# Performance work log

Hardware: AMD Instinct MI355X
Metric: run time of the kernel (lower is better)

## Reference

```python
import jax, jax.numpy as jnp
import numpy as np

THRESH = 0.5
DECAY = 0.99
D = 2048
K = 16384  # memory at full capacity -> static shapes


def _l2norm(x):
    return x / jnp.linalg.norm(x, axis=1, keepdims=True)


def _compute_logits(z, prototypes, temp):
    # temp * <z_hat, p_hat>  -> [1, K]
    return temp[0] * (_l2norm(z) @ _l2norm(prototypes).T)


def setup_inputs() -> dict:
    key = jax.random.key(0)
    k1, k2, k3 = jax.random.split(key, 3)
    z = jax.random.normal(k1, (1, D), dtype=jnp.float32)
    prototypes = jax.random.normal(k2, (K, D), dtype=jnp.float32)
    usages = jax.random.uniform(k3, (K, 1), dtype=jnp.float32, minval=0.1, maxval=1.0)
    beta = jnp.array([-12.0], dtype=jnp.float32)
    gamma = jnp.array([1.0], dtype=jnp.float32)
    temp = jnp.array([10.0], dtype=jnp.float32)
    return {"z": z, "prototypes": prototypes, "usages": usages,
            "beta": beta, "gamma": gamma, "temp": temp}


def reference(z, prototypes, usages, beta, gamma, temp):
    # --- similarity + novelty gate ---
    logits = _compute_logits(z, prototypes, temp)            # [1, K]
    u = jax.nn.sigmoid((-jax.lax.stop_gradient(jnp.max(logits)) - beta[0]) / gamma[0])  # scalar

    def evict_branch(_):
        # remove least-used prototype, append z at the end (shapes stay [K, .])
        idx = jnp.argmin(usages[:, 0])
        pos = jnp.arange(K - 1)
        src = jnp.where(pos < idx, pos, pos + 1)             # skip row idx
        new_p = jnp.concatenate([prototypes[src], z], axis=0)
        new_u = jnp.concatenate([usages[src], jnp.ones((1, 1), usages.dtype)], axis=0)
        return new_p, new_u

    def ema_branch(_):
        y = jax.nn.softmax(logits, axis=1)                   # [1, K]
        delta = (y * (1.0 - u)).T                            # [K, 1]
        new_p = z * (delta / (delta + usages)) + prototypes * (usages / (usages + delta))
        return new_p, usages + delta

    new_protos, new_usages = jax.lax.cond(u >= THRESH, evict_branch, ema_branch, None)
    new_usages = new_usages * DECAY

    # --- final logits / pseudo-label / self cross-entropy ---
    logits2 = _compute_logits(z, new_protos, temp)           # [1, K]
    label = jnp.argmax(logits2, axis=1)                      # [1]
    loss = -jax.nn.log_softmax(logits2, axis=1)[0, label[0]]
    return loss, label, u, new_protos, new_usages
```

## Files before the change

### kernel.cpp

```cpp
#include <hip/hip_runtime.h>
#include <math.h>

#define KP 16384
#define DP 2048
#define THRESH 0.5f
#define DECAY 0.99f


typedef float f4 __attribute__((ext_vector_type(4)));
typedef float f2 __attribute__((ext_vector_type(2)));
typedef unsigned long long u64;

__device__ __forceinline__ float waveReduceSum(float v) {
    #pragma unroll
    for (int m = 32; m >= 1; m >>= 1) v += __shfl_xor(v, m, 64);
    return v;
}

__device__ __forceinline__ unsigned int fkey(float v) {
    unsigned int b = __float_as_uint(v);
    return (b & 0x80000000u) ? ~b : (b | 0x80000000u);
}
__device__ __forceinline__ float fkey_inv(unsigned int key) {
    unsigned int b = (key & 0x80000000u) ? (key ^ 0x80000000u) : ~key;
    return __uint_as_float(b);
}

__global__ __launch_bounds__(1024) void k_argmin(const float* __restrict__ usages,
                                                 float* __restrict__ W) {
    __shared__ u64 s[16];
    const int t = threadIdx.x;
    u64 best = ~0ULL;
    #pragma unroll
    for (int i = 0; i < KP / 1024; i++) {
        const int j = t + i * 1024;
        u64 p = ((u64)fkey(usages[j]) << 32) | (unsigned int)j;
        if (p < best) best = p;
    }
    #pragma unroll
    for (int m = 32; m >= 1; m >>= 1) {
        u64 o = __shfl_xor(best, m, 64);
        if (o < best) best = o;
    }
    if ((t & 63) == 0) s[t >> 6] = best;
    __syncthreads();
    if (t < 64) {
        best = s[t & 15];
        #pragma unroll
        for (int m = 8; m >= 1; m >>= 1) {
            u64 o = __shfl_xor(best, m, 64);
            if (o < best) best = o;
        }
        if (t == 0) ((int*)W)[2] = (int)(best & 0xFFFFFFFFu);
    }
}

__global__ __launch_bounds__(256) void k_dots_copy(const float* __restrict__ z,
                                                   const float* __restrict__ P,
                                                   const float* __restrict__ temp,
                                                   float* __restrict__ W,
                                                   float* __restrict__ out) {
    const int wave = threadIdx.x >> 6;
    const int lane = threadIdx.x & 63;
    const int r = blockIdx.x * 4 + wave;
    const int idx = ((const int*)W)[2];

    const float* prow = P + (size_t)r * DP;

    f4 v[8];
    float zp = 0.f, pp = 0.f, zz = 0.f;
    #pragma unroll
    for (int i = 0; i < 8; i++) {
        const int c = i * 256 + lane * 4;
        const f4 pv = __builtin_nontemporal_load((const f4*)(prow + c));
        const f4 zv = *(const f4*)(z + c);
        v[i] = pv;
        zp += pv.x * zv.x + pv.y * zv.y + pv.z * zv.z + pv.w * zv.w;
        pp += pv.x * pv.x + pv.y * pv.y + pv.z * pv.z + pv.w * pv.w;
        zz += zv.x * zv.x + zv.y * zv.y + zv.z * zv.z + zv.w * zv.w;
    }

    if (r != idx) {
        const int ro = (r < idx) ? r : r - 1;
        float* orow = out + 3 + (size_t)ro * DP;
        if (lane == 0) __builtin_nontemporal_store(v[0].x, orow);
        #pragma unroll
        for (int i = 0; i < 8; i++) {
            float nx = __shfl_down(v[i].x, 1);
            const float bx = __shfl(v[(i + 1) & 7].x, 0);
            if (lane == 63) nx = bx;
            f4 ov;
            ov.x = v[i].y; ov.y = v[i].z; ov.z = v[i].w; ov.w = nx;
            if (i < 7 || lane < 63) {
                __builtin_nontemporal_store(ov, (f4*)(orow + 1 + 4 * (i * 64 + lane)));
            }
        }
        if (lane == 63) {
            f2 t2; t2.x = v[7].y; t2.y = v[7].z;
            __builtin_nontemporal_store(t2, (f2*)(orow + DP - 3));
            __builtin_nontemporal_store(v[7].w, orow + DP - 1);
        }
    }

    zp = waveReduceSum(zp);
    pp = waveReduceSum(pp);
    zz = waveReduceSum(zz);
    if (lane == 0) {
        W[8 + r]          = temp[0] * zp / sqrtf(zz * pp);
        W[8 + KP + r]     = zp;
        W[8 + 2 * KP + r] = pp;
        if (r == 0) W[7] = zz;
    }
}

__global__ __launch_bounds__(1024) void k_scalar(const float* __restrict__ z,
                                                 const float* __restrict__ usages,
                                                 const float* __restrict__ beta,
                                                 const float* __restrict__ gamma,
                                                 const float* __restrict__ temp,
                                                 float* __restrict__ W,
                                                 float* __restrict__ out) {
    __shared__ float sf[1024];
    __shared__ float sm[16];
    __shared__ u64 sb[16];
    const int t = threadIdx.x;
    const int idx = ((const int*)W)[2];

    float lg[KP / 1024];
    float mx_all = -INFINITY;
    u64 bestx = 0;
    #pragma unroll
    for (int i = 0; i < KP / 1024; i++) {
        const int j = t + i * 1024;
        const float v = W[8 + j];
        lg[i] = v;
        mx_all = fmaxf(mx_all, v);
        if (j != idx) {
            u64 p = ((u64)fkey(v) << 32) | (unsigned int)(~j);
            if (p > bestx) bestx = p;
        }
    }
    #pragma unroll
    for (int m = 32; m >= 1; m >>= 1) {
        mx_all = fmaxf(mx_all, __shfl_xor(mx_all, m, 64));
        u64 o = __shfl_xor(bestx, m, 64);
        if (o > bestx) bestx = o;
    }
    if ((t & 63) == 0) { sm[t >> 6] = mx_all; sb[t >> 6] = bestx; }
    __syncthreads();
    if (t < 64) {
        float m = sm[t & 15];
        u64 b = sb[t & 15];
        #pragma unroll
        for (int mk = 8; mk >= 1; mk >>= 1) {
            m = fmaxf(m, __shfl_xor(m, mk, 64));
            u64 o = __shfl_xor(b, mk, 64);
            if (o > b) b = o;
        }
        if (t == 0) { sm[0] = m; sb[0] = b; }
    }
    __syncthreads();
    mx_all = sm[0];

    const float u = 1.f / (1.f + expf(-((-mx_all - beta[0]) / gamma[0])));
    const int flag = (u >= THRESH) ? 1 : 0;
    if (t == 0) {
        out[2] = u;
        ((int*)W)[3] = flag;
        W[4] = mx_all;
        W[6] = u;
    }

    if (flag) {
        const u64 bp = sb[0];
        const float mxe = fkey_inv((unsigned int)(bp >> 32));
        const int amax = (int)(~(unsigned int)(bp & 0xFFFFFFFFu));

        const float tq = temp[0];
        const float M2 = fmaxf(mxe, tq);
        float s = 0.f;
        #pragma unroll
        for (int i = 0; i < KP / 1024; i++) {
            const int j = t + i * 1024;
            if (j != idx) s += expf(lg[i] - M2);
        }
        sf[t] = s;
        __syncthreads();
        for (int off = 512; off >= 1; off >>= 1) {
            if (t < off) sf[t] += sf[t + off];
            __syncthreads();
        }
        if (t == 0) {
            const float total = sf[0] + expf(tq - M2);
            out[0] = logf(total);
            const int label = (mxe >= tq) ? (amax < idx ? amax : amax - 1) : (KP - 1);
            out[1] = (float)label;
        }
        float* ou = out + 3 + (size_t)KP * DP;
        #pragma unroll
        for (int i = 0; i < KP / 1024; i++) {
            const int j = t + i * 1024;
            ou[j] = (j < KP - 1) ? usages[j < idx ? j : j + 1] * DECAY : DECAY;
        }
        float* orow = out + 3 + (size_t)(KP - 1) * DP;
        orow[t] = z[t];
        orow[t + 1024] = z[t + 1024];
    } else {
        float s = 0.f;
        #pragma unroll
        for (int i = 0; i < KP / 1024; i++) s += expf(lg[i] - mx_all);
        sf[t] = s;
        __syncthreads();
        for (int off = 512; off >= 1; off >>= 1) {
            if (t < off) sf[t] += sf[t + off];
            __syncthreads();
        }
        if (t == 0) W[5] = sf[0];
    }
}

__global__ __launch_bounds__(256) void k_ema(const float* __restrict__ z,
                                             const float* __restrict__ P,
                                             const float* __restrict__ usages,
                                             const float* __restrict__ temp,
                                             float* __restrict__ W,
                                             float* __restrict__ out) {
    if (((const int*)W)[3]) return;
    __shared__ float lds[4 * DP];
    const int wave = threadIdx.x >> 6;
    const int lane = threadIdx.x & 63;
    const int r = blockIdx.x * 4 + wave;

    const float mx = W[4], se = W[5], u = W[6], zz = W[7];
    const float lg = W[8 + r], zp = W[8 + KP + r], pp = W[8 + 2 * KP + r];
    const float y = expf(lg - mx) / se;
    const float delta = y * (1.f - u);
    const float usg = usages[r];
    const float a = delta / (delta + usg);
    const float b = usg / (usg + delta);

    const float* prow = P + (size_t)r * DP;
    float* wl = lds + wave * DP;
    float* orow = out + 3 + (size_t)r * DP;
    #pragma unroll
    for (int i = 0; i < 8; i++) {
        const int c = i * 256 + lane * 4;
        const float4 pv = *(const float4*)(prow + c);
        const float4 zv = *(const float4*)(z + c);
        float4 ov;
        ov.x = a * zv.x + b * pv.x;
        ov.y = a * zv.y + b * pv.y;
        ov.z = a * zv.z + b * pv.z;
        ov.w = a * zv.w + b * pv.w;
        *(float4*)(wl + c) = ov;
    }
    #pragma unroll
    for (int j = 0; j < DP / 64; j++) {
        orow[j * 64 + lane] = wl[j * 64 + lane];
    }
    if (lane == 0) {
        const float dzn = a * zz + b * zp;
        const float n2 = a * a * zz + 2.f * a * b * zp + b * b * pp;
        W[8 + 3 * KP + r] = temp[0] * dzn / sqrtf(zz * n2);
        out[3 + (size_t)KP * DP + r] = (usg + delta) * DECAY;
    }
}

__global__ __launch_bounds__(1024) void k_ema_loss(const float* __restrict__ W,
                                                   float* __restrict__ out) {
    if (((const int*)W)[3]) return;
    __shared__ unsigned long long sp[1024];
    __shared__ float sf[1024];
    const int t = threadIdx.x;

    float l2[KP / 1024];
    u64 best = 0;
    #pragma unroll
    for (int i = 0; i < KP / 1024; i++) {
        const int j = t + i * 1024;
        const float v = W[8 + 3 * KP + j];
        l2[i] = v;
        u64 p = ((u64)fkey(v) << 32) | (unsigned int)(~j);
        if (p > best) best = p;
    }
    sp[t] = best;
    __syncthreads();
    for (int off = 512; off >= 1; off >>= 1) {
        if (t < off) { if (sp[t + off] > sp[t]) sp[t] = sp[t + off]; }
        __syncthreads();
    }
    const u64 bp = sp[0];
    const float mx = fkey_inv((unsigned int)(bp >> 32));
    const int label = (int)(~(unsigned int)(bp & 0xFFFFFFFFu));

    float s = 0.f;
    #pragma unroll
    for (int i = 0; i < KP / 1024; i++) s += expf(l2[i] - mx);
    __syncthreads();
    sf[t] = s;
    __syncthreads();
    for (int off = 512; off >= 1; off >>= 1) {
        if (t < off) sf[t] += sf[t + off];
        __syncthreads();
    }
    if (t == 0) {
        out[0] = logf(sf[0]);
        out[1] = (float)label;
    }
}

extern "C" void kernel_launch(void* const* d_in, const int* in_sizes, int n_in,
                              void* d_out, int out_size, void* d_ws, size_t ws_size,
                              hipStream_t stream) {
    const float* z      = (const float*)d_in[0];
    const float* P      = (const float*)d_in[1];
    const float* usages = (const float*)d_in[2];
    const float* beta   = (const float*)d_in[3];
    const float* gamma  = (const float*)d_in[4];
    const float* temp   = (const float*)d_in[5];
    float* out = (float*)d_out;
    float* W   = (float*)d_ws;

    k_argmin<<<1, 1024, 0, stream>>>(usages, W);
    k_dots_copy<<<KP / 4, 256, 0, stream>>>(z, P, temp, W, out);
    k_scalar<<<1, 1024, 0, stream>>>(z, usages, beta, gamma, temp, W, out);
    k_ema<<<KP / 4, 256, 0, stream>>>(z, P, usages, temp, W, out);
    k_ema_loss<<<1, 1024, 0, stream>>>(W, out);
}
```

Before: 253.5 us.

## Fuse scalar and loss reductions into row kernels via last-block atomics

Merges the single-block scalar reduction into the dots/copy kernel and the final loss reduction into the EMA kernel. A global atomic counter picks the last-finishing block, which then runs the reduction. Blocks grow from 4 to 16 rows (1024 threads), and the EMA store drops its LDS staging in favour of shuffle-based, shifted nontemporal stores. The goal is to cut two kernel launches and their serialization gaps. The cost is larger blocks, possible occupancy loss, and re-reading logits from global memory in the tail block.

```diff
diff --git a/kernel.cpp b/kernel.cpp
--- a/kernel.cpp
+++ b/kernel.cpp
@@ -5,6 +5,8 @@
 #define DP 2048
 #define THRESH 0.5f
 #define DECAY 0.99f
+#define ROWS_PER_BLOCK 16
+#define GRID_ROWS (KP / ROWS_PER_BLOCK)
 
 
 typedef float f4 __attribute__((ext_vector_type(4)));
@@ -30,6 +32,7 @@
                                                  float* __restrict__ W) {
     __shared__ u64 s[16];
     const int t = threadIdx.x;
+    if (t == 0) { ((int*)W)[0] = 0; ((int*)W)[1] = 0; }
     u64 best = ~0ULL;
     #pragma unroll
     for (int i = 0; i < KP / 1024; i++) {
@@ -55,14 +58,21 @@
     }
 }
 
-__global__ __launch_bounds__(256) void k_dots_copy(const float* __restrict__ z,
-                                                   const float* __restrict__ P,
-                                                   const float* __restrict__ temp,
-                                                   float* __restrict__ W,
-                                                   float* __restrict__ out) {
+__global__ __launch_bounds__(1024) void k_dots_copy(const float* __restrict__ z,
+                                                    const float* __restrict__ P,
+                                                    const float* __restrict__ usages,
+                                                    const float* __restrict__ beta,
+                                                    const float* __restrict__ gamma,
+                                                    const float* __restrict__ temp,
+                                                    float* __restrict__ W,
+                                                    float* __restrict__ out) {
+    __shared__ float sf[1024];
+    __shared__ float sm[16];
+    __shared__ u64 sb[16];
+    __shared__ int isLast;
     const int wave = threadIdx.x >> 6;
     const int lane = threadIdx.x & 63;
-    const int r = blockIdx.x * 4 + wave;
+    const int r = blockIdx.x * ROWS_PER_BLOCK + wave;
     const int idx = ((const int*)W)[2];
 
     const float* prow = P + (size_t)r * DP;
@@ -111,32 +121,24 @@
         W[8 + 2 * KP + r] = pp;
         if (r == 0) W[7] = zz;
     }
-}
-
-__global__ __launch_bounds__(1024) void k_scalar(const float* __restrict__ z,
-                                                 const float* __restrict__ usages,
-                                                 const float* __restrict__ beta,
-                                                 const float* __restrict__ gamma,
-                                                 const float* __restrict__ temp,
-                                                 float* __restrict__ W,
-                                                 float* __restrict__ out) {
-    __shared__ float sf[1024];
-    __shared__ float sm[16];
-    __shared__ u64 sb[16];
+
+    __threadfence();
+    __syncthreads();
+    if (threadIdx.x == 0) isLast = (atomicAdd((int*)W, 1) == GRID_ROWS - 1);
+    __syncthreads();
+    if (!isLast) return;
+    __threadfence();
+
     const int t = threadIdx.x;
-    const int idx = ((const int*)W)[2];
-
-    float lg[KP / 1024];
     float mx_all = -INFINITY;
     u64 bestx = 0;
     #pragma unroll
     for (int i = 0; i < KP / 1024; i++) {
         const int j = t + i * 1024;
-        const float v = W[8 + j];
-        lg[i] = v;
-        mx_all = fmaxf(mx_all, v);
+        const float v2 = W[8 + j];
+        mx_all = fmaxf(mx_all, v2);
         if (j != idx) {
-            u64 p = ((u64)fkey(v) << 32) | (unsigned int)(~j);
+            u64 p = ((u64)fkey(v2) << 32) | (unsigned int)(~j);
             if (p > bestx) bestx = p;
         }
     }
@@ -182,7 +184,7 @@
         #pragma unroll
         for (int i = 0; i < KP / 1024; i++) {
             const int j = t + i * 1024;
-            if (j != idx) s += expf(lg[i] - M2);
+            if (j != idx) s += expf(W[8 + j] - M2);
         }
         sf[t] = s;
         __syncthreads();
@@ -208,7 +210,7 @@
     } else {
         float s = 0.f;
         #pragma unroll
-        for (int i = 0; i < KP / 1024; i++) s += expf(lg[i] - mx_all);
+        for (int i = 0; i < KP / 1024; i++) s += expf(W[8 + t + i * 1024] - mx_all);
         sf[t] = s;
         __syncthreads();
         for (int off = 512; off >= 1; off >>= 1) {
@@ -219,17 +221,19 @@
     }
 }
 
-__global__ __launch_bounds__(256) void k_ema(const float* __restrict__ z,
-                                             const float* __restrict__ P,
-                                             const float* __restrict__ usages,
-                                             const float* __restrict__ temp,
-                                             float* __restrict__ W,
-                                             float* __restrict__ out) {
+__global__ __launch_bounds__(1024) void k_ema(const float* __restrict__ z,
+                                              const float* __restrict__ P,
+                                              const float* __restrict__ usages,
+                                              const float* __restrict__ temp,
+                                              float* __restrict__ W,
+                                              float* __restrict__ out) {
     if (((const int*)W)[3]) return;
-    __shared__ float lds[4 * DP];
+    __shared__ u64 sp[1024];
+    __shared__ float sfl[1024];
+    __shared__ int isLast;
     const int wave = threadIdx.x >> 6;
     const int lane = threadIdx.x & 63;
-    const int r = blockIdx.x * 4 + wave;
+    const int r = blockIdx.x * ROWS_PER_BLOCK + wave;
 
     const float mx = W[4], se = W[5], u = W[6], zz = W[7];
     const float lg = W[8 + r], zp = W[8 + KP + r], pp = W[8 + 2 * KP + r];
@@ -240,47 +244,61 @@
     const float b = usg / (usg + delta);
 
     const float* prow = P + (size_t)r * DP;
-    float* wl = lds + wave * DP;
     float* orow = out + 3 + (size_t)r * DP;
+    f4 v[8];
     #pragma unroll
     for (int i = 0; i < 8; i++) {
         const int c = i * 256 + lane * 4;
-        const float4 pv = *(const float4*)(prow + c);
-        const float4 zv = *(const float4*)(z + c);
-        float4 ov;
+        const f4 pv = *(const f4*)(prow + c);
+        const f4 zv = *(const f4*)(z + c);
+        f4 ov;
         ov.x = a * zv.x + b * pv.x;
         ov.y = a * zv.y + b * pv.y;
         ov.z = a * zv.z + b * pv.z;
         ov.w = a * zv.w + b * pv.w;
-        *(float4*)(wl + c) = ov;
-    }
-    #pragma unroll
-    for (int j = 0; j < DP / 64; j++) {
-        orow[j * 64 + lane] = wl[j * 64 + lane];
-    }
+        v[i] = ov;
+    }
+    if (lane == 0) __builtin_nontemporal_store(v[0].x, orow);
+    #pragma unroll
+    for (int i = 0; i < 8; i++) {
+        float nx = __shfl_down(v[i].x, 1);
+        const float bx = __shfl(v[(i + 1) & 7].x, 0);
+        if (lane == 63) nx = bx;
+        f4 ov;
+        ov.x = v[i].y; ov.y = v[i].z; ov.z = v[i].w; ov.w = nx;
+        if (i < 7 || lane < 63) {
+            __builtin_nontemporal_store(ov, (f4*)(orow + 1 + 4 * (i * 64 + lane)));
+        }
+    }
+    if (lane == 63) {
+        f2 t2; t2.x = v[7].y; t2.y = v[7].z;
+        __builtin_nontemporal_store(t2, (f2*)(orow + DP - 3));
+        __builtin_nontemporal_store(v[7].w, orow + DP - 1);
+    }
+
     if (lane == 0) {
         const float dzn = a * zz + b * zp;
         const float n2 = a * a * zz + 2.f * a * b * zp + b * b * pp;
         W[8 + 3 * KP + r] = temp[0] * dzn / sqrtf(zz * n2);
         out[3 + (size_t)KP * DP + r] = (usg + delta) * DECAY;
     }
-}
-
-__global__ __launch_bounds__(1024) void k_ema_loss(const float* __restrict__ W,
-                                                   float* __restrict__ out) {
-    if (((const int*)W)[3]) return;
-    __shared__ unsigned long long sp[1024];
-    __shared__ float sf[1024];
+
+    __threadfence();
+    __syncthreads();
+    if (threadIdx.x == 0) isLast = (atomicAdd((int*)W + 1, 1) == GRID_ROWS - 1);
+    __syncthreads();
+    if (!isLast) return;
+    __threadfence();
+
     const int t = threadIdx.x;
-
     float l2[KP / 1024];
     u64 best = 0;
     #pragma unroll
     for (int i = 0; i < KP / 1024; i++) {
         const int j = t + i * 1024;
-        const float v = W[8 + 3 * KP + j];
-        l2[i] = v;
-        u64 p = ((u64)fkey(v) << 32) | (unsigned int)(~j);
+        const float vv = W[8 + 3 * KP + j];
+        l2[i] = vv;
+        u64 p = ((u64)fkey(vv) << 32) | (unsigned int)(~j);
         if (p > best) best = p;
     }
     sp[t] = best;
@@ -290,21 +308,21 @@
         __syncthreads();
     }
     const u64 bp = sp[0];
-    const float mx = fkey_inv((unsigned int)(bp >> 32));
+    const float mxl = fkey_inv((unsigned int)(bp >> 32));
     const int label = (int)(~(unsigned int)(bp & 0xFFFFFFFFu));
 
     float s = 0.f;
     #pragma unroll
-    for (int i = 0; i < KP / 1024; i++) s += expf(l2[i] - mx);
-    __syncthreads();
-    sf[t] = s;
+    for (int i = 0; i < KP / 1024; i++) s += expf(l2[i] - mxl);
+    __syncthreads();
+    sfl[t] = s;
     __syncthreads();
     for (int off = 512; off >= 1; off >>= 1) {
-        if (t < off) sf[t] += sf[t + off];
+        if (t < off) sfl[t] += sfl[t + off];
         __syncthreads();
     }
     if (t == 0) {
-        out[0] = logf(sf[0]);
+        out[0] = logf(sfl[0]);
         out[1] = (float)label;
     }
 }
@@ -322,8 +340,6 @@
     float* W   = (float*)d_ws;
 
     k_argmin<<<1, 1024, 0, stream>>>(usages, W);
-    k_dots_copy<<<KP / 4, 256, 0, stream>>>(z, P, temp, W, out);
-    k_scalar<<<1, 1024, 0, stream>>>(z, usages, beta, gamma, temp, W, out);
-    k_ema<<<KP / 4, 256, 0, stream>>>(z, P, usages, temp, W, out);
-    k_ema_loss<<<1, 1024, 0, stream>>>(W, out);
-}
+    k_dots_copy<<<GRID_ROWS, 1024, 0, stream>>>(z, P, usages, beta, gamma, temp, W, out);
+    k_ema<<<GRID_ROWS, 1024, 0, stream>>>(z, P, usages, temp, W, out);
+}
```

After: 919.7 us. 263% more time.
